# Performance work log

Measured on AMD Instinct MI355X. Metric: run time of the kernel, lower is better.

The kernel has to match this reference:

```python
import jax, jax.numpy as jnp
import numpy as np

NUM_EXPERTS = 8
TOP_K = 2
D_MODEL = 1024
D_HID = 4096
BATCH, SEQ = 2, 2048


def setup_inputs() -> dict:
    key = jax.random.key(0)
    ks = jax.random.split(key, 5)
    s = 0.02  # param scale
    return {
        "x": jax.random.normal(ks[0], (BATCH, SEQ, D_MODEL), dtype=jnp.float32),
        "Wg": jax.random.normal(ks[1], (D_MODEL, NUM_EXPERTS), dtype=jnp.float32) * s,
        "bg": jnp.zeros((NUM_EXPERTS,), dtype=jnp.float32),
        "W0": jax.random.normal(ks[2], (NUM_EXPERTS, D_MODEL, D_HID), dtype=jnp.float32) * s,
        "b0": jnp.zeros((NUM_EXPERTS, D_HID), dtype=jnp.float32),
        "W1": jax.random.normal(ks[3], (NUM_EXPERTS, D_MODEL, D_HID), dtype=jnp.float32) * s,
        "b1": jnp.zeros((NUM_EXPERTS, D_HID), dtype=jnp.float32),
        "W2": jax.random.normal(ks[4], (NUM_EXPERTS, D_HID, D_MODEL), dtype=jnp.float32) * s,
        "b2": jnp.zeros((NUM_EXPERTS, D_MODEL), dtype=jnp.float32),
    }


def reference(x, Wg, bg, W0, b0, W1, b1, W2, b2):
    n, s, d = x.shape
    # --- routing ---
    gate_logits = x @ Wg + bg                      # [n, s, E]
    top_vals, top_idx = jax.lax.top_k(gate_logits, TOP_K)  # [n, s, K]
    w = jax.nn.softmax(top_vals, axis=-1)          # [n, s, K]
    # combine weights scattered back to dense [n, s, E]
    combine = jnp.sum(jax.nn.one_hot(top_idx, NUM_EXPERTS, dtype=x.dtype) * w[..., None], axis=-2)
    # --- dense expert compute (all experts on all tokens, masked combine) ---
    xf = x.reshape(n * s, d)                       # [T, d]
    h = jnp.einsum('td,edh->eth', xf, W0) + b0[:, None, :]   # [E, T, H]
    g = jax.nn.silu(jnp.einsum('td,edh->eth', xf, W1) + b1[:, None, :])
    y = jnp.einsum('eth,ehd->etd', h * g, W2) + b2[:, None, :]  # [E, T, d]
    out = jnp.einsum('te,etd->td', combine.reshape(n * s, NUM_EXPERTS), y)
    return out.reshape(n, s, d)
```

## Files before the change

kernel.cpp:

```cpp
#include <hip/hip_runtime.h>

#define NTOK 4096
#define DM 1024
#define DH 4096
#define NE 8

typedef __attribute__((ext_vector_type(8))) short bf16x8;
typedef __attribute__((ext_vector_type(4))) float f32x4;
typedef __attribute__((ext_vector_type(8))) unsigned short u16x8;

__device__ __forceinline__ ushort f2bf(float f) {
  union { float f; unsigned u; } v; v.f = f;
  unsigned r = v.u + 0x7fffu + ((v.u >> 16) & 1u);
  return (ushort)(r >> 16);
}

#define GL2LDS(g, l) __builtin_amdgcn_global_load_lds( \
    (__attribute__((address_space(1))) const void*)(g), \
    (__attribute__((address_space(3))) void*)(l), 16, 0, 0)

__global__ __launch_bounds__(256) void gate_kernel(
    const float* __restrict__ x, const float* __restrict__ Wg,
    const float* __restrict__ bg, int* __restrict__ tkE,
    float* __restrict__ tkW, int* __restrict__ gcnt)
{
  const int wave = threadIdx.x >> 6;
  const int lane = threadIdx.x & 63;
  const int t = blockIdx.x * 4 + wave;

  float acc[NE];
#pragma unroll
  for (int e = 0; e < NE; e++) acc[e] = 0.f;

  for (int i = 0; i < DM / 64; i++) {
    int d = i * 64 + lane;
    float xv = x[(long)t * DM + d];
#pragma unroll
    for (int e = 0; e < NE; e++) acc[e] += xv * Wg[d * NE + e];
  }
#pragma unroll
  for (int e = 0; e < NE; e++) {
#pragma unroll
    for (int off = 32; off; off >>= 1) acc[e] += __shfl_xor(acc[e], off, 64);
    acc[e] += bg[e];
  }
  int e0 = 0; float v0 = acc[0];
#pragma unroll
  for (int e = 1; e < NE; e++) if (acc[e] > v0) { v0 = acc[e]; e0 = e; }
  int e1 = -1; float v1 = -3.4e38f;
#pragma unroll
  for (int e = 0; e < NE; e++) if (e != e0 && acc[e] > v1) { v1 = acc[e]; e1 = e; }
  float w0 = 1.f / (1.f + __expf(v1 - v0));
  float w1 = 1.f - w0;
  if (lane == 0) {
    tkE[t] = e0 | (e1 << 8);
    tkW[2 * t] = w0;
    tkW[2 * t + 1] = w1;
    atomicAdd(&gcnt[e0], 1);
    atomicAdd(&gcnt[e1], 1);
  }
}

__global__ void scan_kernel(const int* __restrict__ gcnt, int* __restrict__ offs,
                            int* __restrict__ cursor)
{
  if (threadIdx.x == 0) {
    int o = 0;
    for (int e = 0; e < NE; e++) { offs[e] = o; o += gcnt[e]; cursor[e] = 0; }
    offs[NE] = o;
  }
}

__global__ __launch_bounds__(256) void build_kernel(
    const int* __restrict__ tkE, const float* __restrict__ tkW,
    const int* __restrict__ offs, int* __restrict__ cursor,
    int* __restrict__ rmeta, float* __restrict__ rw)
{
  int t = blockIdx.x * 256 + threadIdx.x;
  int ee = tkE[t];
#pragma unroll
  for (int k = 0; k < 2; k++) {
    int e = (k == 0) ? (ee & 0xff) : (ee >> 8);
    int pos = atomicAdd(&cursor[e], 1);
    int row = offs[e] + pos;
    rmeta[row] = t * 2 + k;
    rw[row] = tkW[t * 2 + k];
  }
}

__global__ __launch_bounds__(256) void gather_kernel(
    const float* __restrict__ x, const int* __restrict__ rmeta,
    ushort* __restrict__ xg)
{
  int row = blockIdx.x;
  int t = rmeta[row] >> 1;
  const float4* src = (const float4*)(x + (long)t * DM);
  float4 v = src[threadIdx.x];
  ushort4 o = { f2bf(v.x), f2bf(v.y), f2bf(v.z), f2bf(v.w) };
  *(ushort4*)(xg + (long)row * DM + threadIdx.x * 4) = o;
}

__global__ __launch_bounds__(256) void transpose_cvt(
    const float* __restrict__ src, ushort* __restrict__ dst,
    int R, int C, long srcE, long dstE)
{
  __shared__ __align__(16) float tile[64][68];
  const int e = blockIdx.z;
  const int r0 = blockIdx.y * 64;
  const int c0 = blockIdx.x * 64;
  const float* s = src + (long)e * srcE;
  ushort* d = dst + (long)e * dstE;
  const int tid = threadIdx.x;
  const int lr = tid >> 4;
  const int lc4 = tid & 15;
#pragma unroll
  for (int p = 0; p < 4; p++) {
    int r = p * 16 + lr;
    float4 v = *(const float4*)&s[(long)(r0 + r) * C + c0 + lc4 * 4];
    *(float4*)&tile[r][lc4 * 4] = v;
  }
  __syncthreads();
  const int oc = tid >> 2;
  const int seg = tid & 3;
  u16x8 o0, o1;
#pragma unroll
  for (int j = 0; j < 8; j++) {
    o0[j] = f2bf(tile[seg * 8 + j][oc]);
    o1[j] = f2bf(tile[32 + seg * 8 + j][oc]);
  }
  ushort* dp = &d[(long)(c0 + oc) * R + r0];
  *(u16x8*)(dp + seg * 8) = o0;
  *(u16x8*)(dp + 32 + seg * 8) = o1;
}

__global__ __launch_bounds__(256, 3) void gemm1_kernel(
    const ushort* __restrict__ xg, const ushort* __restrict__ Wt01,
    const float* __restrict__ b0, const float* __restrict__ b1,
    const int* __restrict__ offs, ushort* __restrict__ aout)
{
  const int flat = blockIdx.x + 16 * (blockIdx.y + 64 * blockIdx.z);
  const int xcd = flat & 7;
  const int s_ = flat >> 3;
  const int mt = s_ & 15;
  const int grp = s_ >> 4;
  const int gid = grp * 8 + xcd;
  const int e = gid >> 6;
  const int nt = gid & 63;

  const int off_e = offs[e];
  const int cnt = offs[e + 1] - off_e;
  if (mt * 128 >= cnt) return;
  const int nbase = nt * 64;

  __shared__ ushort As[128 * 32];
  __shared__ ushort Bh[64 * 32];
  __shared__ ushort Bg[64 * 32];

  const int tid = threadIdx.x;
  const int wave = tid >> 6;
  const int lane = tid & 63;
  const int wm = wave & 1;
  const int wn = wave >> 1;

  const ushort* Ap = xg + (long)(off_e + mt * 128) * DM;
  const ushort* Bhp = Wt01 + (long)e * (2 * DH) * DM + (long)nbase * DM;
  const ushort* Bgp = Bhp + (long)DH * DM;

  f32x4 acc_h[4][2], acc_g[4][2];
#pragma unroll
  for (int i = 0; i < 4; i++)
#pragma unroll
    for (int j = 0; j < 2; j++) {
      acc_h[i][j] = (f32x4){0.f, 0.f, 0.f, 0.f};
      acc_g[i][j] = (f32x4){0.f, 0.f, 0.f, 0.f};
    }

  const int soff0 = wave * 1024 + lane * 16;

  for (int k0 = 0; k0 < DM; k0 += 32) {
    __syncthreads();
    {
#pragma unroll
      for (int s = 0; s < 2; s++) {
        int off = s * 4096 + soff0;
        int r = off >> 6;
        int ie = (off & 63) >> 1;
        GL2LDS(Ap + (long)r * DM + k0 + ie, (char*)As + off);
      }
      int r = soff0 >> 6;
      int ie = (soff0 & 63) >> 1;
      GL2LDS(Bhp + (long)r * DM + k0 + ie, (char*)Bh + soff0);
      GL2LDS(Bgp + (long)r * DM + k0 + ie, (char*)Bg + soff0);
    }
    __syncthreads();

    bf16x8 af[4], bhf[2], bgf[2];
#pragma unroll
    for (int i = 0; i < 4; i++) {
      int ro = (wm * 64 + i * 16 + (lane & 15)) * 32 + (lane >> 4) * 8;
      af[i] = *(const bf16x8*)&As[ro];
    }
#pragma unroll
    for (int j = 0; j < 2; j++) {
      int rb = (wn * 32 + j * 16 + (lane & 15)) * 32 + (lane >> 4) * 8;
      bhf[j] = *(const bf16x8*)&Bh[rb];
      bgf[j] = *(const bf16x8*)&Bg[rb];
    }
#pragma unroll
    for (int i = 0; i < 4; i++)
#pragma unroll
      for (int j = 0; j < 2; j++) {
        acc_h[i][j] = __builtin_amdgcn_mfma_f32_16x16x32_bf16(af[i], bhf[j], acc_h[i][j], 0, 0, 0);
        acc_g[i][j] = __builtin_amdgcn_mfma_f32_16x16x32_bf16(af[i], bgf[j], acc_g[i][j], 0, 0, 0);
      }
  }

#pragma unroll
  for (int j = 0; j < 2; j++) {
    const int col = nbase + wn * 32 + j * 16 + (lane & 15);
    const float bb0 = b0[e * DH + col];
    const float bb1 = b1[e * DH + col];
#pragma unroll
    for (int i = 0; i < 4; i++) {
#pragma unroll
      for (int r = 0; r < 4; r++) {
        int mlocal = mt * 128 + wm * 64 + i * 16 + (lane >> 4) * 4 + r;
        if (mlocal < cnt) {
          float h = acc_h[i][j][r] + bb0;
          float g = acc_g[i][j][r] + bb1;
          float a = h * (g / (1.f + __expf(-g)));
          aout[(long)(off_e + mlocal) * DH + col] = f2bf(a);
        }
      }
    }
  }
}

__global__ __launch_bounds__(256, 3) void gemm2_kernel(
    const ushort* __restrict__ aout, const ushort* __restrict__ W2t,
    const int* __restrict__ offs, const int* __restrict__ rmeta,
    const float* __restrict__ rw, float* __restrict__ ybuf)
{
  const int flat = blockIdx.x + 16 * (blockIdx.y + 16 * blockIdx.z);
  const int xcd = flat & 7;
  const int s_ = flat >> 3;
  const int mt = s_ & 15;
  const int grp = s_ >> 4;
  const int gid = grp * 8 + xcd;
  const int e = gid >> 4;
  const int rest = gid & 15;
  const int nt = rest >> 1;
  const int kc = rest & 1;

  const int off_e = offs[e];
  const int cnt = offs[e + 1] - off_e;
  if (mt * 128 >= cnt) return;
  const int nbase = nt * 128;

  __shared__ ushort As[128 * 32];
  __shared__ ushort Bs[128 * 32];

  const int tid = threadIdx.x;
  const int wave = tid >> 6;
  const int lane = tid & 63;
  const int wm = wave & 1;
  const int wn = wave >> 1;

  const ushort* Ap = aout + (long)(off_e + mt * 128) * DH;
  const ushort* Bp = W2t + (long)e * DM * DH + (long)nbase * DH;

  f32x4 acc[4][4];
#pragma unroll
  for (int i = 0; i < 4; i++)
#pragma unroll
    for (int j = 0; j < 4; j++) acc[i][j] = (f32x4){0.f, 0.f, 0.f, 0.f};

  const int soff0 = wave * 1024 + lane * 16;
  const int kbase = kc * 2048;

  for (int k0 = kbase; k0 < kbase + 2048; k0 += 32) {
    __syncthreads();
#pragma unroll
    for (int s = 0; s < 2; s++) {
      int off = s * 4096 + soff0;
      int r = off >> 6;
      int ie = (off & 63) >> 1;
      long gelem = (long)r * DH + k0 + ie;
      GL2LDS(Ap + gelem, (char*)As + off);
      GL2LDS(Bp + gelem, (char*)Bs + off);
    }
    __syncthreads();

    bf16x8 af[4], bfr[4];
#pragma unroll
    for (int i = 0; i < 4; i++) {
      int ro = (i * 16 + (lane & 15)) * 32 + (lane >> 4) * 8;
      af[i]  = *(const bf16x8*)&As[(wm * 64) * 32 + ro];
      bfr[i] = *(const bf16x8*)&Bs[(wn * 64) * 32 + ro];
    }
#pragma unroll
    for (int i = 0; i < 4; i++)
#pragma unroll
      for (int j = 0; j < 4; j++)
        acc[i][j] = __builtin_amdgcn_mfma_f32_16x16x32_bf16(af[i], bfr[j], acc[i][j], 0, 0, 0);
  }

#pragma unroll
  for (int j = 0; j < 4; j++) {
    const int col = nbase + wn * 64 + j * 16 + (lane & 15);
#pragma unroll
    for (int i = 0; i < 4; i++) {
#pragma unroll
      for (int r = 0; r < 4; r++) {
        int mlocal = mt * 128 + wm * 64 + i * 16 + (lane >> 4) * 4 + r;
        if (mlocal < cnt) {
          int grow = off_e + mlocal;
          ybuf[((long)kc * 8192 + rmeta[grow]) * DM + col] = rw[grow] * acc[i][j][r];
        }
      }
    }
  }
}

__global__ __launch_bounds__(256) void combine_kernel(
    const float* __restrict__ ybuf, const int* __restrict__ tkE,
    const float* __restrict__ tkW, const float* __restrict__ b2,
    float* __restrict__ out)
{
  const int t = blockIdx.x;
  const int c = threadIdx.x * 4;
  const int ee = tkE[t];
  const int e0 = ee & 0xff, e1 = ee >> 8;
  const float w0 = tkW[2 * t], w1 = tkW[2 * t + 1];

  float4 acc = {0.f, 0.f, 0.f, 0.f};
#pragma unroll
  for (int kc = 0; kc < 2; kc++) {
#pragma unroll
    for (int k = 0; k < 2; k++) {
      const float4 v = *(const float4*)&ybuf[((long)kc * 8192 + 2 * t + k) * DM + c];
      acc.x += v.x; acc.y += v.y; acc.z += v.z; acc.w += v.w;
    }
  }
  const float4 p0 = *(const float4*)&b2[(long)e0 * DM + c];
  const float4 p1 = *(const float4*)&b2[(long)e1 * DM + c];
  acc.x += w0 * p0.x + w1 * p1.x;
  acc.y += w0 * p0.y + w1 * p1.y;
  acc.z += w0 * p0.z + w1 * p1.z;
  acc.w += w0 * p0.w + w1 * p1.w;
  *(float4*)&out[(long)t * DM + c] = acc;
}

extern "C" void kernel_launch(void* const* d_in, const int* in_sizes, int n_in,
                              void* d_out, int out_size, void* d_ws, size_t ws_size,
                              hipStream_t stream) {
  const float* x  = (const float*)d_in[0];
  const float* Wg = (const float*)d_in[1];
  const float* bg = (const float*)d_in[2];
  const float* W0 = (const float*)d_in[3];
  const float* b0 = (const float*)d_in[4];
  const float* W1 = (const float*)d_in[5];
  const float* b1 = (const float*)d_in[6];
  const float* W2 = (const float*)d_in[7];
  const float* b2 = (const float*)d_in[8];
  float* out = (float*)d_out;

  char* ws = (char*)d_ws;
  ushort* Wt01 = (ushort*)(ws + 0);
  float*  ybuf = (float*)(ws + 0);
  ushort* W2t  = (ushort*)(ws + 134217728);
  ushort* xg   = (ushort*)(ws + 201326592);
  ushort* aout = (ushort*)(ws + 218365952);
  int*    tkE  = (int*)(ws + 320077824);
  float*  tkW  = (float*)(ws + 320094208);
  int*    rmeta= (int*)(ws + 320126976);
  float*  rw   = (float*)(ws + 320160256);
  int*    gcnt = (int*)(ws + 320193536);
  int*    offs = gcnt + 8;
  int*    cursor = gcnt + 20;

  hipMemsetAsync(gcnt, 0, 32, stream);
  gate_kernel<<<NTOK / 4, 256, 0, stream>>>(x, Wg, bg, tkE, tkW, gcnt);
  scan_kernel<<<1, 64, 0, stream>>>(gcnt, offs, cursor);
  build_kernel<<<NTOK / 256, 256, 0, stream>>>(tkE, tkW, offs, cursor, rmeta, rw);
  gather_kernel<<<2 * NTOK, 256, 0, stream>>>(x, rmeta, xg);

  transpose_cvt<<<dim3(64, 16, 8), 256, 0, stream>>>(
      W0, Wt01, 1024, 4096, (long)1024 * 4096, (long)8192 * 1024);
  transpose_cvt<<<dim3(64, 16, 8), 256, 0, stream>>>(
      W1, Wt01 + (long)4096 * 1024, 1024, 4096, (long)1024 * 4096, (long)8192 * 1024);
  transpose_cvt<<<dim3(16, 64, 8), 256, 0, stream>>>(
      W2, W2t, 4096, 1024, (long)4096 * 1024, (long)1024 * 4096);

  gemm1_kernel<<<dim3(16, 64, 8), 256, 0, stream>>>(xg, Wt01, b0, b1, offs, aout);
  gemm2_kernel<<<dim3(16, 16, 8), 256, 0, stream>>>(aout, W2t, offs, rmeta, rw, ybuf);
  combine_kernel<<<dim3(NTOK), 256, 0, stream>>>(ybuf, tkE, tkW, b2, out);
}
```

Measured before the change: 926.3 us.

## Enlarge expert GEMM tiles with double-buffered swizzled LDS pipeline

Both expert GEMMs move to 512-thread blocks with larger output tiles: 256x128 (times two for the h and g halves) in gemm1, and 256x256 in gemm2. The K step grows to 64, and two LDS buffers are filled asynchronously with global-to-LDS loads, gated by explicit vmcnt waits, so the next stage loads while the current one computes. An XOR swizzle on the LDS layout is meant to avoid bank conflicts, and s_setprio is raised around the MFMA bursts. This should cut global traffic per FLOP and hide load latency, in exchange for about 128KB of LDS per block and heavy accumulator register pressure that may cause spills or limit occupancy.

```diff
diff --git a/kernel.cpp b/kernel.cpp
--- a/kernel.cpp
+++ b/kernel.cpp
@@ -133,101 +133,128 @@
   *(u16x8*)(dp + 32 + seg * 8) = o1;
 }
 
-__global__ __launch_bounds__(256, 3) void gemm1_kernel(
+__global__ __launch_bounds__(512, 2) void gemm1_kernel(
     const ushort* __restrict__ xg, const ushort* __restrict__ Wt01,
     const float* __restrict__ b0, const float* __restrict__ b1,
     const int* __restrict__ offs, ushort* __restrict__ aout)
 {
-  const int flat = blockIdx.x + 16 * (blockIdx.y + 64 * blockIdx.z);
+  const int flat = blockIdx.x;
   const int xcd = flat & 7;
-  const int s_ = flat >> 3;
-  const int mt = s_ & 15;
-  const int grp = s_ >> 4;
-  const int gid = grp * 8 + xcd;
-  const int e = gid >> 6;
-  const int nt = gid & 63;
+  const int rest = flat >> 3;
+  const int mt = rest & 7;
+  const int g2 = rest >> 3;
+  const int val = g2 * 8 + xcd;
+  const int e = val >> 5;
+  const int nt = val & 31;
 
   const int off_e = offs[e];
   const int cnt = offs[e + 1] - off_e;
-  if (mt * 128 >= cnt) return;
-  const int nbase = nt * 64;
-
-  __shared__ ushort As[128 * 32];
-  __shared__ ushort Bh[64 * 32];
-  __shared__ ushort Bg[64 * 32];
+  if (mt * 256 >= cnt) return;
+  const int nbase = nt * 128;
+
+  __shared__ ushort As[2 * 256 * 64];
+  __shared__ ushort Bh[2 * 128 * 64];
+  __shared__ ushort Bg[2 * 128 * 64];
 
   const int tid = threadIdx.x;
+  const int lane = tid & 63;
   const int wave = tid >> 6;
-  const int lane = tid & 63;
-  const int wm = wave & 1;
-  const int wn = wave >> 1;
-
-  const ushort* Ap = xg + (long)(off_e + mt * 128) * DM;
+  const int wm = wave & 3;
+  const int wn = wave >> 2;
+
+  const ushort* Ap = xg + (long)(off_e + mt * 256) * DM;
   const ushort* Bhp = Wt01 + (long)e * (2 * DH) * DM + (long)nbase * DM;
   const ushort* Bgp = Bhp + (long)DH * DM;
 
-  f32x4 acc_h[4][2], acc_g[4][2];
+  f32x4 acc_h[4][4], acc_g[4][4];
 #pragma unroll
   for (int i = 0; i < 4; i++)
 #pragma unroll
-    for (int j = 0; j < 2; j++) {
+    for (int j = 0; j < 4; j++) {
       acc_h[i][j] = (f32x4){0.f, 0.f, 0.f, 0.f};
       acc_g[i][j] = (f32x4){0.f, 0.f, 0.f, 0.f};
     }
 
-  const int soff0 = wave * 1024 + lane * 16;
-
-  for (int k0 = 0; k0 < DM; k0 += 32) {
-    __syncthreads();
-    {
-#pragma unroll
-      for (int s = 0; s < 2; s++) {
-        int off = s * 4096 + soff0;
-        int r = off >> 6;
-        int ie = (off & 63) >> 1;
-        GL2LDS(Ap + (long)r * DM + k0 + ie, (char*)As + off);
-      }
-      int r = soff0 >> 6;
-      int ie = (soff0 & 63) >> 1;
-      GL2LDS(Bhp + (long)r * DM + k0 + ie, (char*)Bh + soff0);
-      GL2LDS(Bgp + (long)r * DM + k0 + ie, (char*)Bg + soff0);
-    }
-    __syncthreads();
-
-    bf16x8 af[4], bhf[2], bgf[2];
-#pragma unroll
-    for (int i = 0; i < 4; i++) {
-      int ro = (wm * 64 + i * 16 + (lane & 15)) * 32 + (lane >> 4) * 8;
-      af[i] = *(const bf16x8*)&As[ro];
-    }
-#pragma unroll
-    for (int j = 0; j < 2; j++) {
-      int rb = (wn * 32 + j * 16 + (lane & 15)) * 32 + (lane >> 4) * 8;
-      bhf[j] = *(const bf16x8*)&Bh[rb];
-      bgf[j] = *(const bf16x8*)&Bg[rb];
-    }
-#pragma unroll
-    for (int i = 0; i < 4; i++)
-#pragma unroll
-      for (int j = 0; j < 2; j++) {
-        acc_h[i][j] = __builtin_amdgcn_mfma_f32_16x16x32_bf16(af[i], bhf[j], acc_h[i][j], 0, 0, 0);
-        acc_g[i][j] = __builtin_amdgcn_mfma_f32_16x16x32_bf16(af[i], bgf[j], acc_g[i][j], 0, 0, 0);
-      }
-  }
-
-#pragma unroll
-  for (int j = 0; j < 2; j++) {
-    const int col = nbase + wn * 32 + j * 16 + (lane & 15);
+  auto stage = [&](int cur, int k0) {
+#pragma unroll
+    for (int s = 0; s < 4; s++) {
+      int loff = s * 8192 + tid * 16;
+      int row = loff >> 7;
+      int sg = ((loff >> 4) & 7) ^ (row & 7);
+      GL2LDS(Ap + (long)row * DM + k0 + sg * 8, (char*)As + cur * 32768 + loff);
+    }
+#pragma unroll
+    for (int s = 0; s < 2; s++) {
+      int loff = s * 8192 + tid * 16;
+      int row = loff >> 7;
+      int sg = ((loff >> 4) & 7) ^ (row & 7);
+      GL2LDS(Bhp + (long)row * DM + k0 + sg * 8, (char*)Bh + cur * 16384 + loff);
+      GL2LDS(Bgp + (long)row * DM + k0 + sg * 8, (char*)Bg + cur * 16384 + loff);
+    }
+  };
+
+  stage(0, 0);
+  stage(1, 64);
+
+  for (int t = 0; t < 16; t++) {
+    const int cur = t & 1;
+    if (t < 15) asm volatile("s_waitcnt vmcnt(8)" ::: "memory");
+    else        asm volatile("s_waitcnt vmcnt(0)" ::: "memory");
+    __builtin_amdgcn_s_barrier();
+    asm volatile("" ::: "memory");
+
+    const char* Ab  = (const char*)As + cur * 32768;
+    const char* Bhb = (const char*)Bh + cur * 16384;
+    const char* Bgb = (const char*)Bg + cur * 16384;
+
+    bf16x8 af[4][2];
+#pragma unroll
+    for (int mi = 0; mi < 4; mi++)
+#pragma unroll
+      for (int ks = 0; ks < 2; ks++) {
+        int row = wm * 64 + mi * 16 + (lane & 15);
+        int seg = ks * 4 + (lane >> 4);
+        af[mi][ks] = *(const bf16x8*)(Ab + row * 128 + ((seg ^ (row & 7)) << 4));
+      }
+#pragma unroll
+    for (int j = 0; j < 4; j++) {
+      bf16x8 bh[2], bg[2];
+#pragma unroll
+      for (int ks = 0; ks < 2; ks++) {
+        int row = wn * 64 + j * 16 + (lane & 15);
+        int seg = ks * 4 + (lane >> 4);
+        int o = row * 128 + ((seg ^ (row & 7)) << 4);
+        bh[ks] = *(const bf16x8*)(Bhb + o);
+        bg[ks] = *(const bf16x8*)(Bgb + o);
+      }
+      __builtin_amdgcn_s_setprio(1);
+#pragma unroll
+      for (int mi = 0; mi < 4; mi++) {
+        acc_h[mi][j] = __builtin_amdgcn_mfma_f32_16x16x32_bf16(af[mi][0], bh[0], acc_h[mi][j], 0, 0, 0);
+        acc_h[mi][j] = __builtin_amdgcn_mfma_f32_16x16x32_bf16(af[mi][1], bh[1], acc_h[mi][j], 0, 0, 0);
+        acc_g[mi][j] = __builtin_amdgcn_mfma_f32_16x16x32_bf16(af[mi][0], bg[0], acc_g[mi][j], 0, 0, 0);
+        acc_g[mi][j] = __builtin_amdgcn_mfma_f32_16x16x32_bf16(af[mi][1], bg[1], acc_g[mi][j], 0, 0, 0);
+      }
+      __builtin_amdgcn_s_setprio(0);
+      __builtin_amdgcn_s_barrier();
+    }
+    asm volatile("" ::: "memory");
+    if (t + 2 < 16) stage(cur, (t + 2) * 64);
+  }
+
+#pragma unroll
+  for (int j = 0; j < 4; j++) {
+    const int col = nbase + wn * 64 + j * 16 + (lane & 15);
     const float bb0 = b0[e * DH + col];
     const float bb1 = b1[e * DH + col];
 #pragma unroll
-    for (int i = 0; i < 4; i++) {
+    for (int mi = 0; mi < 4; mi++) {
 #pragma unroll
       for (int r = 0; r < 4; r++) {
-        int mlocal = mt * 128 + wm * 64 + i * 16 + (lane >> 4) * 4 + r;
+        int mlocal = mt * 256 + wm * 64 + mi * 16 + (lane >> 4) * 4 + r;
         if (mlocal < cnt) {
-          float h = acc_h[i][j][r] + bb0;
-          float g = acc_g[i][j][r] + bb1;
+          float h = acc_h[mi][j][r] + bb0;
+          float g = acc_g[mi][j][r] + bb1;
           float a = h * (g / (1.f + __expf(-g)));
           aout[(long)(off_e + mlocal) * DH + col] = f2bf(a);
         }
@@ -236,86 +263,113 @@
   }
 }
 
-__global__ __launch_bounds__(256, 3) void gemm2_kernel(
+__global__ __launch_bounds__(512, 2) void gemm2_kernel(
     const ushort* __restrict__ aout, const ushort* __restrict__ W2t,
     const int* __restrict__ offs, const int* __restrict__ rmeta,
     const float* __restrict__ rw, float* __restrict__ ybuf)
 {
-  const int flat = blockIdx.x + 16 * (blockIdx.y + 16 * blockIdx.z);
+  const int flat = blockIdx.x;
   const int xcd = flat & 7;
-  const int s_ = flat >> 3;
-  const int mt = s_ & 15;
-  const int grp = s_ >> 4;
-  const int gid = grp * 8 + xcd;
-  const int e = gid >> 4;
-  const int rest = gid & 15;
-  const int nt = rest >> 1;
-  const int kc = rest & 1;
+  const int rest = flat >> 3;
+  const int mt = rest & 7;
+  const int g2 = rest >> 3;
+  const int val = g2 * 8 + xcd;
+  const int e = val >> 3;
+  const int r2 = val & 7;
+  const int nt = r2 >> 1;
+  const int kc = r2 & 1;
 
   const int off_e = offs[e];
   const int cnt = offs[e + 1] - off_e;
-  if (mt * 128 >= cnt) return;
-  const int nbase = nt * 128;
-
-  __shared__ ushort As[128 * 32];
-  __shared__ ushort Bs[128 * 32];
+  if (mt * 256 >= cnt) return;
+  const int nbase = nt * 256;
+  const int kbase = kc * 2048;
+
+  __shared__ ushort As[2 * 256 * 64];
+  __shared__ ushort Bs[2 * 256 * 64];
 
   const int tid = threadIdx.x;
+  const int lane = tid & 63;
   const int wave = tid >> 6;
-  const int lane = tid & 63;
   const int wm = wave & 1;
   const int wn = wave >> 1;
 
-  const ushort* Ap = aout + (long)(off_e + mt * 128) * DH;
+  const ushort* Ap = aout + (long)(off_e + mt * 256) * DH;
   const ushort* Bp = W2t + (long)e * DM * DH + (long)nbase * DH;
 
-  f32x4 acc[4][4];
-#pragma unroll
-  for (int i = 0; i < 4; i++)
+  f32x4 acc[8][4];
+#pragma unroll
+  for (int i = 0; i < 8; i++)
 #pragma unroll
     for (int j = 0; j < 4; j++) acc[i][j] = (f32x4){0.f, 0.f, 0.f, 0.f};
 
-  const int soff0 = wave * 1024 + lane * 16;
-  const int kbase = kc * 2048;
-
-  for (int k0 = kbase; k0 < kbase + 2048; k0 += 32) {
-    __syncthreads();
-#pragma unroll
-    for (int s = 0; s < 2; s++) {
-      int off = s * 4096 + soff0;
-      int r = off >> 6;
-      int ie = (off & 63) >> 1;
-      long gelem = (long)r * DH + k0 + ie;
-      GL2LDS(Ap + gelem, (char*)As + off);
-      GL2LDS(Bp + gelem, (char*)Bs + off);
-    }
-    __syncthreads();
-
-    bf16x8 af[4], bfr[4];
-#pragma unroll
-    for (int i = 0; i < 4; i++) {
-      int ro = (i * 16 + (lane & 15)) * 32 + (lane >> 4) * 8;
-      af[i]  = *(const bf16x8*)&As[(wm * 64) * 32 + ro];
-      bfr[i] = *(const bf16x8*)&Bs[(wn * 64) * 32 + ro];
-    }
-#pragma unroll
-    for (int i = 0; i < 4; i++)
-#pragma unroll
-      for (int j = 0; j < 4; j++)
-        acc[i][j] = __builtin_amdgcn_mfma_f32_16x16x32_bf16(af[i], bfr[j], acc[i][j], 0, 0, 0);
+  auto stage = [&](int cur, int k0) {
+#pragma unroll
+    for (int s = 0; s < 4; s++) {
+      int loff = s * 8192 + tid * 16;
+      int row = loff >> 7;
+      int sg = ((loff >> 4) & 7) ^ (row & 7);
+      long gelem = (long)row * DH + k0 + sg * 8;
+      GL2LDS(Ap + gelem, (char*)As + cur * 32768 + loff);
+      GL2LDS(Bp + gelem, (char*)Bs + cur * 32768 + loff);
+    }
+  };
+
+  stage(0, kbase);
+  stage(1, kbase + 64);
+
+  for (int t = 0; t < 32; t++) {
+    const int cur = t & 1;
+    if (t < 31) asm volatile("s_waitcnt vmcnt(8)" ::: "memory");
+    else        asm volatile("s_waitcnt vmcnt(0)" ::: "memory");
+    __builtin_amdgcn_s_barrier();
+    asm volatile("" ::: "memory");
+
+    const char* Ab = (const char*)As + cur * 32768;
+    const char* Bb = (const char*)Bs + cur * 32768;
+
+    bf16x8 af[8][2];
+#pragma unroll
+    for (int mi = 0; mi < 8; mi++)
+#pragma unroll
+      for (int ks = 0; ks < 2; ks++) {
+        int row = wm * 128 + mi * 16 + (lane & 15);
+        int seg = ks * 4 + (lane >> 4);
+        af[mi][ks] = *(const bf16x8*)(Ab + row * 128 + ((seg ^ (row & 7)) << 4));
+      }
+#pragma unroll
+    for (int j = 0; j < 4; j++) {
+      bf16x8 bf2[2];
+#pragma unroll
+      for (int ks = 0; ks < 2; ks++) {
+        int row = wn * 64 + j * 16 + (lane & 15);
+        int seg = ks * 4 + (lane >> 4);
+        bf2[ks] = *(const bf16x8*)(Bb + row * 128 + ((seg ^ (row & 7)) << 4));
+      }
+      __builtin_amdgcn_s_setprio(1);
+#pragma unroll
+      for (int mi = 0; mi < 8; mi++) {
+        acc[mi][j] = __builtin_amdgcn_mfma_f32_16x16x32_bf16(af[mi][0], bf2[0], acc[mi][j], 0, 0, 0);
+        acc[mi][j] = __builtin_amdgcn_mfma_f32_16x16x32_bf16(af[mi][1], bf2[1], acc[mi][j], 0, 0, 0);
+      }
+      __builtin_amdgcn_s_setprio(0);
+      __builtin_amdgcn_s_barrier();
+    }
+    asm volatile("" ::: "memory");
+    if (t + 2 < 32) stage(cur, kbase + (t + 2) * 64);
   }
 
 #pragma unroll
   for (int j = 0; j < 4; j++) {
     const int col = nbase + wn * 64 + j * 16 + (lane & 15);
 #pragma unroll
-    for (int i = 0; i < 4; i++) {
+    for (int mi = 0; mi < 8; mi++) {
 #pragma unroll
       for (int r = 0; r < 4; r++) {
-        int mlocal = mt * 128 + wm * 64 + i * 16 + (lane >> 4) * 4 + r;
+        int mlocal = mt * 256 + wm * 128 + mi * 16 + (lane >> 4) * 4 + r;
         if (mlocal < cnt) {
           int grow = off_e + mlocal;
-          ybuf[((long)kc * 8192 + rmeta[grow]) * DM + col] = rw[grow] * acc[i][j][r];
+          ybuf[((long)kc * 8192 + rmeta[grow]) * DM + col] = rw[grow] * acc[mi][j][r];
         }
       }
     }
@@ -370,12 +424,12 @@
   float*  ybuf = (float*)(ws + 0);
   ushort* W2t  = (ushort*)(ws + 134217728);
   ushort* xg   = (ushort*)(ws + 201326592);
-  ushort* aout = (ushort*)(ws + 218365952);
-  int*    tkE  = (int*)(ws + 320077824);
-  float*  tkW  = (float*)(ws + 320094208);
-  int*    rmeta= (int*)(ws + 320126976);
-  float*  rw   = (float*)(ws + 320160256);
-  int*    gcnt = (int*)(ws + 320193536);
+  ushort* aout = (ushort*)(ws + 218628096);
+  int*    tkE  = (int*)(ws + 287834112);
+  float*  tkW  = (float*)(ws + 287850496);
+  int*    rmeta= (int*)(ws + 287883264);
+  float*  rw   = (float*)(ws + 287916032);
+  int*    gcnt = (int*)(ws + 287948800);
   int*    offs = gcnt + 8;
   int*    cursor = gcnt + 20;
 
@@ -392,7 +446,7 @@
   transpose_cvt<<<dim3(16, 64, 8), 256, 0, stream>>>(
       W2, W2t, 4096, 1024, (long)4096 * 1024, (long)1024 * 4096);
 
-  gemm1_kernel<<<dim3(16, 64, 8), 256, 0, stream>>>(xg, Wt01, b0, b1, offs, aout);
-  gemm2_kernel<<<dim3(16, 16, 8), 256, 0, stream>>>(aout, W2t, offs, rmeta, rw, ybuf);
+  gemm1_kernel<<<2048, 512, 0, stream>>>(xg, Wt01, b0, b1, offs, aout);
+  gemm2_kernel<<<512, 512, 0, stream>>>(aout, W2t, offs, rmeta, rw, ybuf);
   combine_kernel<<<dim3(NTOK), 256, 0, stream>>>(ybuf, tkE, tkW, b2, out);
 }
```

New measurement: 1.079 ms. 1.16x slower.
